# Kernel optimization log

Measured on AMD Instinct MI355X. Metric: run time of the kernel, lower is better.

## Reference

```python
import jax, jax.numpy as jnp
import numpy as np

B, N, D = 32, 4096, 256
S = 8            # num_slots
H = 512          # mlp hidden (max(dim, hidden_dim))
EPS = 1e-8
LN_EPS = 1e-5


def _ln(x, w, b):
    m = x.mean(-1, keepdims=True)
    v = ((x - m) ** 2).mean(-1, keepdims=True)
    return (x - m) / jnp.sqrt(v + LN_EPS) * w + b


def _gru_cell(x, h, wih, whh, bih, bhh):
    # torch.nn.GRUCell math; wih/whh: [3D, D], bih/bhh: [3D]
    gi = x @ wih.T + bih
    gh = h @ whh.T + bhh
    i_r, i_z, i_n = jnp.split(gi, 3, axis=-1)
    h_r, h_z, h_n = jnp.split(gh, 3, axis=-1)
    r = jax.nn.sigmoid(i_r + h_r)
    z = jax.nn.sigmoid(i_z + h_z)
    n = jnp.tanh(i_n + r * h_n)
    return (1.0 - z) * n + z * h


def setup_inputs() -> dict:
    key = jax.random.key(0)
    ks = jax.random.split(key, 24)
    f = jnp.float32
    p = lambda k, shp, s=0.02: (jax.random.normal(k, shp, dtype=f) * s)
    inp = {
        "x": jax.random.normal(ks[0], (B, N, D), dtype=f),
        "slots_noise": jax.random.normal(ks[1], (B, S, D), dtype=f),
        "num_iterations": 3,
        "slots_mu": jax.random.normal(ks[2], (1, 1, D), dtype=f),
        "slots_sigma": jax.random.normal(ks[3], (1, 1, D), dtype=f),
        "wq": p(ks[4], (D, D)), "bq": jnp.zeros((D,), f),
        "wk": p(ks[5], (D, D)), "bk": jnp.zeros((D,), f),
        "wv": p(ks[6], (D, D)), "bv": jnp.zeros((D,), f),
        "gru_wih": p(ks[7], (3 * D, D)), "gru_whh": p(ks[8], (3 * D, D)),
        "gru_bih": jnp.zeros((3 * D,), f), "gru_bhh": jnp.zeros((3 * D,), f),
        "fc1_w": p(ks[9], (H, D)), "fc1_b": jnp.zeros((H,), f),
        "fc2_w": p(ks[10], (D, H)), "fc2_b": jnp.zeros((D,), f),
        "ln_in_w": jnp.ones((D,), f), "ln_in_b": jnp.zeros((D,), f),
        "ln_sl_w": jnp.ones((D,), f), "ln_sl_b": jnp.zeros((D,), f),
        "ln_ff_w": jnp.ones((D,), f), "ln_ff_b": jnp.zeros((D,), f),
    }
    return inp


def reference(x, slots_noise, num_iterations, slots_mu, slots_sigma,
              wq, bq, wk, bk, wv, bv,
              gru_wih, gru_whh, gru_bih, gru_bhh,
              fc1_w, fc1_b, fc2_w, fc2_b,
              ln_in_w, ln_in_b, ln_sl_w, ln_sl_b, ln_ff_w, ln_ff_b):
    b, n, d = x.shape
    scale = d ** (-0.5)
    slots = slots_mu + slots_sigma * slots_noise          # [B,S,D]
    xn = _ln(x, ln_in_w, ln_in_b)
    k = xn @ wk.T + bk                                    # [B,N,D]
    v = xn @ wv.T + bv                                    # [B,N,D]
    for _ in range(num_iterations):
        slots_prev = slots
        s = _ln(slots, ln_sl_w, ln_sl_b)
        q = s @ wq.T + bq                                 # [B,S,D]
        dots = jnp.einsum('bid,bjd->bij', q, k) * scale   # [B,S,N]
        attn = jax.nn.softmax(dots, axis=1) + EPS         # softmax over SLOT axis
        attn = attn / attn.sum(axis=-1, keepdims=True)
        updates = jnp.einsum('bjd,bij->bid', v, attn)     # [B,S,D]
        slots = _gru_cell(updates.reshape(-1, d), slots_prev.reshape(-1, d),
                          gru_wih, gru_whh, gru_bih, gru_bhh).reshape(b, -1, d)
        ff = jax.nn.relu(_ln(slots, ln_ff_w, ln_ff_b) @ fc1_w.T + fc1_b) @ fc2_w.T + fc2_b
        slots = slots + ff
    return slots
```

## Files before the change

kernel.cpp:

```cpp
#include <hip/hip_runtime.h>
#include <hip/hip_fp16.h>
#include <math.h>

#define NB 32
#define NTOK 4096
#define DIM 256
#define NS 8
#define HID 512
#define NCHUNK 32
#define LN_EPS 1e-5f
#define ATT_EPS 1e-8f
#define SCALE 0.0625f
#define NROWS (NB * NS)

#define DPPF(x, ctrl) __int_as_float(__builtin_amdgcn_update_dpp(0, __float_as_int(x), (ctrl), 0xF, 0xF, true))

__device__ __forceinline__ float addx16(float c) {
#if __has_builtin(__builtin_amdgcn_permlane16_swap)
    auto r = __builtin_amdgcn_permlane16_swap(__float_as_uint(c), __float_as_uint(c), false, false);
    return __uint_as_float(r[0]) + __uint_as_float(r[1]);
#else
    return c + __shfl_xor(c, 16);
#endif
}
__device__ __forceinline__ float addx32(float c) {
#if __has_builtin(__builtin_amdgcn_permlane32_swap)
    auto r = __builtin_amdgcn_permlane32_swap(__float_as_uint(c), __float_as_uint(c), false, false);
    return __uint_as_float(r[0]) + __uint_as_float(r[1]);
#else
    return c + __shfl_xor(c, 32);
#endif
}

__device__ __forceinline__ void tree2(float v0, float v1, int lane, float& S, float& Q) {
    bool hi = lane & 1;
    float send = hi ? v0 : v1;
    float recv = DPPF(send, 0xB1);
    float a = (hi ? v1 : v0) + recv;
    a += DPPF(a, 0x4E);
    a += DPPF(a, 0x124);
    a += DPPF(a, 0x128);
    a = addx16(a);
    a = addx32(a);
    float other = DPPF(a, 0xB1);
    S = hi ? other : a;
    Q = hi ? a : other;
}

__device__ __forceinline__ float tree8h(const float v[8], int lane) {
    bool b0 = lane & 1;
    bool b1 = lane & 2;
    bool bp = ((lane ^ (lane >> 1) ^ (lane >> 2)) & 1);
    float a[4];
#pragma unroll
    for (int j = 0; j < 4; j++) {
        float send = b0 ? v[j] : v[4 + j];
        float recv = DPPF(send, 0xB1);
        a[j] = (b0 ? v[4 + j] : v[j]) + recv;
    }
    float b[2];
#pragma unroll
    for (int j = 0; j < 2; j++) {
        float send = b1 ? a[j] : a[2 + j];
        float recv = DPPF(send, 0x4E);
        b[j] = (b1 ? a[2 + j] : a[j]) + recv;
    }
    float send = bp ? b[0] : b[1];
    float recv = DPPF(send, 0x141);
    float c = (bp ? b[1] : b[0]) + recv;
    c += DPPF(c, 0x128);
    c = addx16(c);
    return c;
}

typedef _Float16 h2v __attribute__((ext_vector_type(2)));
__device__ __forceinline__ float fdot2u(unsigned a, unsigned b, float c) {
#if __has_builtin(__builtin_amdgcn_fdot2)
    return __builtin_amdgcn_fdot2(__builtin_bit_cast(h2v, a), __builtin_bit_cast(h2v, b), c, false);
#else
    __half2 ha = __builtin_bit_cast(__half2, a), hb = __builtin_bit_cast(__half2, b);
    return c + __low2float(ha) * __low2float(hb) + __high2float(ha) * __high2float(hb);
#endif
}
__device__ __forceinline__ unsigned pkh(float a, float b) {
    return __builtin_bit_cast(unsigned, __floats2half2_rn(a, b));
}
__device__ __forceinline__ float2 h2f2(unsigned u) {
    __half2 h = __builtin_bit_cast(__half2, u);
    return float2{__low2float(h), __high2float(h)};
}

#define WP_BIAS  128
#define WP_WHH0  129
#define WP_F1H0  225
#define WP_F2H0  289
#define WP_W2C0  353
#define WP_F1B0  401
#define WP_B2G0  403
#define WP_BLKS  406

__global__ void __launch_bounds__(256)
k_wprep(const float* __restrict__ wq, const float* __restrict__ wk,
        const float* __restrict__ bk, const float* __restrict__ bq,
        const float* __restrict__ lsb, const float* __restrict__ lsw,
        unsigned* __restrict__ MppH, float* __restrict__ u2p, float* __restrict__ biasp,
        const float* __restrict__ wv, const float* __restrict__ wih,
        unsigned* __restrict__ w2cH,
        const float* __restrict__ f1w, const float* __restrict__ f1b,
        const float* __restrict__ lfb, float* __restrict__ f1bp,
        const float* __restrict__ bih, const float* __restrict__ bv,
        float* __restrict__ b2g,
        const float* __restrict__ whh, const float* __restrict__ f2w,
        const float* __restrict__ lfw,
        unsigned* __restrict__ whhH, unsigned* __restrict__ f1H,
        unsigned* __restrict__ f2H) {
    int bid = blockIdx.x, t = threadIdx.x;

    if (bid < WP_BIAS) {
        int b = bid, o = t;
        float a0 = 0.f, a1 = 0.f;
        for (int d = 0; d < 256; d++) {
            float2 wqp = *(const float2*)&wq[(size_t)d * 256 + 2 * b];
            float wkv = wk[(size_t)d * 256 + o];
            a0 = fmaf(wqp.x, wkv, a0);
            a1 = fmaf(wqp.y, wkv, a1);
        }
        MppH[(size_t)b * 256 + o] = pkh(a0 * lsw[2 * b], a1 * lsw[2 * b + 1]);
        return;
    }
    if (bid == WP_BIAS) {
        int o = t;
        __shared__ float t2l[256], bkl[256], red[4];
        bkl[o] = bk[o];
        float a = bq[o];
        for (int k = 0; k < 256; k++) a = fmaf(wq[(size_t)o * 256 + k], lsb[k], a);
        t2l[o] = a;
        __syncthreads();
        float ab = 0.f, au = 0.f;
        for (int d = 0; d < 256; d++) {
            ab = fmaf(t2l[d], wk[(size_t)d * 256 + o], ab);
            au = fmaf(bkl[d], wq[(size_t)d * 256 + o], au);
        }
        biasp[o] = ab;
        u2p[o] = au * lsw[o];
        float kk = t2l[o] * bkl[o];
        kk += DPPF(kk, 0xB1);
        kk += DPPF(kk, 0x4E);
        kk += DPPF(kk, 0x124);
        kk += DPPF(kk, 0x128);
        kk = addx16(kk);
        kk = addx32(kk);
        if ((t & 63) == 0) red[t >> 6] = kk;
        __syncthreads();
        if (t == 0) biasp[256] = red[0] + red[1] + red[2] + red[3];
        return;
    }
    if (bid < WP_W2C0) {
        const float* in; unsigned* out; const float* scl = nullptr;
        int C, OS, r, RT;
        if (bid < WP_F1H0)      { in = whh; out = whhH; C = 256; OS = 768; r = bid - WP_WHH0; RT = 24; }
        else if (bid < WP_F2H0) { in = f1w; out = f1H;  C = 256; OS = 512; r = bid - WP_F1H0; RT = 16; scl = lfw; }
        else                    { in = f2w; out = f2H;  C = 512; OS = 256; r = bid - WP_F2H0; RT = 8; }
        int otl = r % RT, ept = r / RT;
        __shared__ float tile[32][65];
#pragma unroll
        for (int i = 0; i < 8; i++) {
            int idx = t + i * 256;
            int row = idx >> 6, col = idx & 63;
            tile[row][col] = in[(size_t)(otl * 32 + row) * C + ept * 64 + col];
        }
        __syncthreads();
#pragma unroll
        for (int i = 0; i < 4; i++) {
            int idx = t + i * 256;
            int epl = idx >> 5, ol = idx & 31;
            float v0 = tile[ol][2 * epl], v1 = tile[ol][2 * epl + 1];
            if (scl) { v0 *= scl[ept * 64 + 2 * epl]; v1 *= scl[ept * 64 + 2 * epl + 1]; }
            out[(size_t)(ept * 32 + epl) * OS + otl * 32 + ol] = pkh(v0, v1);
        }
        return;
    }
    if (bid < WP_F1B0) {
        int r = bid - WP_W2C0;
        int et = r & 3, ot = r >> 2;
        int ep = et * 32 + (t & 31), og = (t >> 5) * 8;
        float alo[8] = {}, ahi[8] = {};
        for (int d = 0; d < 256; d++) {
            float2 wvp = *(const float2*)&wv[(size_t)d * 256 + 2 * ep];
#pragma unroll
            for (int i = 0; i < 8; i++) {
                float wv_ih = wih[(size_t)(ot * 64 + og + i) * 256 + d];
                alo[i] = fmaf(wvp.x, wv_ih, alo[i]);
                ahi[i] = fmaf(wvp.y, wv_ih, ahi[i]);
            }
        }
#pragma unroll
        for (int i = 0; i < 8; i++)
            w2cH[(size_t)ep * 768 + ot * 64 + og + i] = pkh(alo[i], ahi[i]);
        return;
    }
    if (bid < WP_B2G0) {
        int h = (bid - WP_F1B0) * 256 + t;
        float a = f1b[h];
        for (int e = 0; e < 256; e++) a = fmaf(f1w[(size_t)h * 256 + e], lfb[e], a);
        f1bp[h] = a;
        return;
    }
    {
        int o = (bid - WP_B2G0) * 256 + t;
        float a = bih[o];
        for (int d = 0; d < 256; d++) a = fmaf(wih[(size_t)o * 256 + d], bv[d], a);
        b2g[o] = a;
    }
}

__global__ void __launch_bounds__(256)
k_xn(const float* __restrict__ x, const float* __restrict__ liw,
     const float* __restrict__ lib, __half* __restrict__ xh) {
    int bid = blockIdx.x, t = threadIdx.x;
    int wave = t >> 6, lane = t & 63;
    float4 w4 = *(const float4*)&liw[lane * 4];
    float4 b4 = *(const float4*)&lib[lane * 4];
    size_t rbase = (size_t)bid * 64 + wave;
    float4 cur = *(const float4*)&x[rbase * 256 + lane * 4];
    for (int i = 0; i < 16; i++) {
        float4 nxt;
        if (i < 15) nxt = *(const float4*)&x[(rbase + (size_t)(i + 1) * 4) * 256 + lane * 4];
        float S, Q;
        tree2(cur.x + cur.y + cur.z + cur.w,
              cur.x * cur.x + cur.y * cur.y + cur.z * cur.z + cur.w * cur.w, lane, S, Q);
        float m = S * (1.f / DIM);
        float rstd = rsqrtf(Q * (1.f / DIM) - m * m + LN_EPS);
        uint2 st;
        st.x = pkh((cur.x - m) * rstd * w4.x + b4.x, (cur.y - m) * rstd * w4.y + b4.y);
        st.y = pkh((cur.z - m) * rstd * w4.z + b4.z, (cur.w - m) * rstd * w4.w + b4.w);
        *(uint2*)&xh[(rbase + (size_t)i * 4) * 256 + lane * 4] = st;
        cur = nxt;
    }
}

__global__ void __launch_bounds__(512)
k_iq(const float* __restrict__ noise, const float* __restrict__ mu,
     const float* __restrict__ sg, float* __restrict__ slots,
     const unsigned* __restrict__ MppH, const float* __restrict__ biasp,
     const float* __restrict__ u2p,
     float* __restrict__ qkw, float* __restrict__ c2b) {
    int bb = blockIdx.x, t = threadIdx.x, wave = t >> 6, lane = t & 63;
    __shared__ float S2[NS][DIM], Zl[NS][DIM];
#pragma unroll
    for (int k = 0; k < 4; k++) {
        int idx = k * 512 + t, d = idx & 255;
        float v = mu[d] + sg[d] * noise[(size_t)bb * 2048 + idx];
        S2[idx >> 8][d] = v;
        slots[(size_t)bb * 2048 + idx] = v;
    }
    __syncthreads();
    {
        float4 xv = *(const float4*)&S2[wave][lane * 4];
        float S, Q;
        tree2(xv.x + xv.y + xv.z + xv.w,
              xv.x * xv.x + xv.y * xv.y + xv.z * xv.z + xv.w * xv.w, lane, S, Q);
        float m = S * (1.f / DIM);
        float rstd = rsqrtf(Q * (1.f / DIM) - m * m + LN_EPS);
        Zl[wave][lane * 4 + 0] = (xv.x - m) * rstd;
        Zl[wave][lane * 4 + 1] = (xv.y - m) * rstd;
        Zl[wave][lane * 4 + 2] = (xv.z - m) * rstd;
        Zl[wave][lane * 4 + 3] = (xv.w - m) * rstd;
    }
    __syncthreads();
    int o = t & 255, sg2 = (t >> 8) * 4;
    float acc[4] = {};
    for (int ep = 0; ep < 128; ep++) {
        float2 wf = h2f2(MppH[(size_t)ep * 256 + o]);
#pragma unroll
        for (int i = 0; i < 4; i++) {
            float2 zp = *(const float2*)&Zl[sg2 + i][2 * ep];
            acc[i] = fmaf(zp.x, wf.x, fmaf(zp.y, wf.y, acc[i]));
        }
    }
    float bo = biasp[o];
#pragma unroll
    for (int i = 0; i < 4; i++)
        qkw[(size_t)(bb * NS + sg2 + i) * DIM + o] = acc[i] + bo;
    if (t < 64) {
        int s = t >> 3, j = t & 7;
        float a = 0.f;
        for (int e = j * 32; e < j * 32 + 32; e++) a = fmaf(Zl[s][e], u2p[e], a);
        a += DPPF(a, 0xB1);
        a += DPPF(a, 0x4E);
        a += DPPF(a, 0x141);
        if (j == 0) c2b[bb * NS + s] = a + biasp[256];
    }
}

__global__ void __launch_bounds__(256, 3)
k_attn(const __half* __restrict__ xh, const float* __restrict__ qkw,
       const float* __restrict__ c2b,
       float* __restrict__ pu, float* __restrict__ pda) {
    const int bb = blockIdx.x, chunk = blockIdx.y;
    const int t = threadIdx.x, wave = t >> 6, lane = t & 63;
    const int l0 = lane & 1, l1 = (lane >> 1) & 1, l2 = (lane >> 2) & 1;
    const int sig = (l0 << 2) | (l1 << 1) | (l0 ^ l1 ^ l2);
    const int e0 = (lane & 31) * 8;

    unsigned qh[NS][4];
#pragma unroll
    for (int s = 0; s < NS; s++) {
        const float4 a = *(const float4*)&qkw[(size_t)(bb * NS + s) * DIM + e0];
        const float4 b = *(const float4*)&qkw[(size_t)(bb * NS + s) * DIM + e0 + 4];
        qh[s][0] = pkh(a.x, a.y); qh[s][1] = pkh(a.z, a.w);
        qh[s][2] = pkh(b.x, b.y); qh[s][3] = pkh(b.z, b.w);
    }
    const float qbs = c2b[bb * NS + sig] * SCALE;

    float ua[NS][8] = {};
    float da[NS] = {};

    const __half* xp = xh + ((size_t)bb * NTOK + chunk * 128 + wave * 32 + (lane >> 5)) * DIM + e0;
    uint4 nxt = *(const uint4*)xp;
    for (int i = 0; i < 16; i++) {
        uint4 xv = nxt;
        if (i < 15) nxt = *(const uint4*)(xp + (size_t)(i + 1) * 2 * DIM);
        float dp[NS];
#pragma unroll
        for (int s = 0; s < NS; s++)
            dp[s] = fdot2u(qh[s][0], xv.x, fdot2u(qh[s][1], xv.y,
                    fdot2u(qh[s][2], xv.z, fdot2u(qh[s][3], xv.w, 0.f))));
        float ds = tree8h(dp, lane);
        float dv = fmaf(ds, SCALE, qbs);
        float mx = dv;
        mx = fmaxf(mx, DPPF(mx, 0xB1));
        mx = fmaxf(mx, DPPF(mx, 0x4E));
        mx = fmaxf(mx, DPPF(mx, 0x141));
        float e = __expf(dv - mx);
        float sm = e;
        sm += DPPF(sm, 0xB1);
        sm += DPPF(sm, 0x4E);
        sm += DPPF(sm, 0x141);
        float g0 = fmaf(e, __fdividef(1.f, sm), ATT_EPS);
        float g1 = DPPF(g0, 0x141);
        float g2 = DPPF(g0, 0x4E);
        float g3 = DPPF(g1, 0x4E);
        float g4 = DPPF(g0, 0xB1);
        float g5 = DPPF(g1, 0xB1);
        float g6 = DPPF(g2, 0xB1);
        float g7 = DPPF(g3, 0xB1);
        float gth[NS] = {g0, g1, g2, g3, g4, g5, g6, g7};
        __half2 p0 = __builtin_bit_cast(__half2, xv.x);
        __half2 p1 = __builtin_bit_cast(__half2, xv.y);
        __half2 p2 = __builtin_bit_cast(__half2, xv.z);
        __half2 p3 = __builtin_bit_cast(__half2, xv.w);
        float xf[8] = {__low2float(p0), __high2float(p0), __low2float(p1), __high2float(p1),
                       __low2float(p2), __high2float(p2), __low2float(p3), __high2float(p3)};
#pragma unroll
        for (int j = 0; j < NS; j++) {
            float pj = gth[j];
            da[j] += pj;
#pragma unroll
            for (int k = 0; k < 8; k++) ua[j][k] = fmaf(pj, xf[k], ua[j][k]);
        }
    }
#pragma unroll
    for (int j = 0; j < NS; j++) {
        da[j] = addx32(da[j]);
#pragma unroll
        for (int k = 0; k < 8; k++) ua[j][k] = addx32(ua[j][k]);
    }
    __shared__ float ul[4][NS][DIM];
    __shared__ float dl[4][NS];
    const int M8[NS] = {0, 7, 3, 4, 5, 2, 6, 1};
    if (lane < 32) {
#pragma unroll
        for (int j = 0; j < NS; j++) {
            int sj = sig ^ M8[j];
            *(float4*)&ul[wave][sj][e0]     = float4{ua[j][0], ua[j][1], ua[j][2], ua[j][3]};
            *(float4*)&ul[wave][sj][e0 + 4] = float4{ua[j][4], ua[j][5], ua[j][6], ua[j][7]};
        }
    }
    if (lane < 8) {
#pragma unroll
        for (int j = 0; j < NS; j++) dl[wave][sig ^ M8[j]] = da[j];
    }
    __syncthreads();
    size_t base = ((size_t)bb * NCHUNK + chunk) * NS;
#pragma unroll
    for (int s = 0; s < NS; s++)
        pu[(base + s) * DIM + t] = ul[0][s][t] + ul[1][s][t] + ul[2][s][t] + ul[3][s][t];
    if (t < NS)
        pda[base + t] = dl[0][t] + dl[1][t] + dl[2][t] + dl[3][t];
}

__global__ void __launch_bounds__(256)
k_fin(const float* __restrict__ pu, const float* __restrict__ pda,
      float* __restrict__ Aavg) {
    int bb = blockIdx.x, s = blockIdx.y, t = threadIdx.x;
    __shared__ float dsh;
    if (t < 64) {
        float a = pda[((size_t)bb * NCHUNK + (t & 31)) * NS + s];
        a += DPPF(a, 0xB1);
        a += DPPF(a, 0x4E);
        a += DPPF(a, 0x124);
        a += DPPF(a, 0x128);
        a = addx16(a);
        if (t == 0) dsh = a;
    }
    const float* src = pu + ((size_t)bb * NCHUNK * NS + s) * DIM + t;
    float acc = 0.f;
#pragma unroll 8
    for (int c = 0; c < NCHUNK; c++) acc += src[(size_t)c * NS * DIM];
    __syncthreads();
    Aavg[((size_t)bb * NS + s) * DIM + t] = acc * __fdividef(1.f, dsh);
}

__global__ void __launch_bounds__(512)
k_gru(const float* __restrict__ Aavg, const float* __restrict__ slots,
      const unsigned* __restrict__ w2cH, const unsigned* __restrict__ whhH,
      const float* __restrict__ b2g, const float* __restrict__ bhh,
      float* __restrict__ news) {
    int bb = blockIdx.x, ot = blockIdx.y, t = threadIdx.x;
    __shared__ unsigned AlH[NS][128], SlH[NS][128];
    __shared__ float pp[7][64][24];
    for (int idx = t; idx < 1024; idx += 512) {
        int rr = idx >> 7, pi = idx & 127;
        float2 av = *(const float2*)&Aavg[(size_t)bb * 2048 + rr * 256 + 2 * pi];
        float2 sv = *(const float2*)&slots[(size_t)bb * 2048 + rr * 256 + 2 * pi];
        AlH[rr][pi] = pkh(av.x, av.y);
        SlH[rr][pi] = pkh(sv.x, sv.y);
    }
    __syncthreads();
    int q = t & 7, r = (t >> 3) & 7, kp = t >> 6;
    int oc0 = ot * 32 + q * 4;
    float ir[4] = {}, iz[4] = {}, in_[4] = {}, hr[4] = {}, hz[4] = {}, hn[4] = {};
    int p0 = kp * 16;
#pragma unroll 4
    for (int i = 0; i < 16; i++) {
        int ep = p0 + i;
        uint4 w0 = *(const uint4*)&w2cH[(size_t)ep * 768 + oc0];
        uint4 w1 = *(const uint4*)&w2cH[(size_t)ep * 768 + oc0 + 256];
        uint4 w2 = *(const uint4*)&w2cH[(size_t)ep * 768 + oc0 + 512];
        uint4 u0 = *(const uint4*)&whhH[(size_t)ep * 768 + oc0];
        uint4 u1 = *(const uint4*)&whhH[(size_t)ep * 768 + oc0 + 256];
        uint4 u2 = *(const uint4*)&whhH[(size_t)ep * 768 + oc0 + 512];
        unsigned ah = AlH[r][ep], hh = SlH[r][ep];
        const unsigned* w0u = (const unsigned*)&w0;
        const unsigned* w1u = (const unsigned*)&w1;
        const unsigned* w2u = (const unsigned*)&w2;
        const unsigned* u0u = (const unsigned*)&u0;
        const unsigned* u1u = (const unsigned*)&u1;
        const unsigned* u2u = (const unsigned*)&u2;
#pragma unroll
        for (int j = 0; j < 4; j++) {
            ir[j]  = fdot2u(w0u[j], ah, ir[j]);
            iz[j]  = fdot2u(w1u[j], ah, iz[j]);
            in_[j] = fdot2u(w2u[j], ah, in_[j]);
            hr[j]  = fdot2u(u0u[j], hh, hr[j]);
            hz[j]  = fdot2u(u1u[j], hh, hz[j]);
            hn[j]  = fdot2u(u2u[j], hh, hn[j]);
        }
    }
    int slot = (r << 3) | q;
    if (kp) {
        float* d = &pp[kp - 1][slot][0];
#pragma unroll
        for (int j = 0; j < 4; j++) {
            d[j] = ir[j]; d[4 + j] = iz[j]; d[8 + j] = in_[j];
            d[12 + j] = hr[j]; d[16 + j] = hz[j]; d[20 + j] = hn[j];
        }
    }
    __syncthreads();
    if (!kp) {
#pragma unroll
        for (int k = 0; k < 7; k++) {
            const float* s_ = &pp[k][slot][0];
#pragma unroll
            for (int j = 0; j < 4; j++) {
                ir[j] += s_[j]; iz[j] += s_[4 + j]; in_[j] += s_[8 + j];
                hr[j] += s_[12 + j]; hz[j] += s_[16 + j]; hn[j] += s_[20 + j];
            }
        }
        float4 hv = *(const float4*)&slots[((size_t)bb * NS + r) * DIM + oc0];
        float hvv[4] = {hv.x, hv.y, hv.z, hv.w};
        float out[4];
#pragma unroll
        for (int j = 0; j < 4; j++) {
            int oc = oc0 + j;
            float gir = ir[j] + b2g[oc], giz = iz[j] + b2g[oc + 256], gin = in_[j] + b2g[oc + 512];
            float ghr = hr[j] + bhh[oc], ghz = hz[j] + bhh[oc + 256], ghn = hn[j] + bhh[oc + 512];
            float rg = 1.f / (1.f + __expf(-(gir + ghr)));
            float zg = 1.f / (1.f + __expf(-(giz + ghz)));
            float ng = tanhf(fmaf(rg, ghn, gin));
            out[j] = fmaf(zg, hvv[j] - ng, ng);
        }
        *(float4*)&news[((size_t)bb * NS + r) * DIM + oc0] = float4{out[0], out[1], out[2], out[3]};
    }
}

__global__ void __launch_bounds__(512)
k_ff1(const float* __restrict__ news, const unsigned* __restrict__ f1H,
      const float* __restrict__ f1bp, unsigned* __restrict__ h1H) {
    int bb = blockIdx.x, ht = blockIdx.y, t = threadIdx.x;
    int wave = t >> 6, lane = t & 63;
    __shared__ unsigned ZH[NS][128];
    __shared__ float pp[3][128][4];
    {
        float4 xv = *(const float4*)&news[((size_t)bb * NS + wave) * DIM + lane * 4];
        float S, Q;
        tree2(xv.x + xv.y + xv.z + xv.w,
              xv.x * xv.x + xv.y * xv.y + xv.z * xv.z + xv.w * xv.w, lane, S, Q);
        float m = S * (1.f / DIM);
        float rstd = rsqrtf(Q * (1.f / DIM) - m * m + LN_EPS);
        ZH[wave][lane * 2]     = pkh((xv.x - m) * rstd, (xv.y - m) * rstd);
        ZH[wave][lane * 2 + 1] = pkh((xv.z - m) * rstd, (xv.w - m) * rstd);
    }
    __syncthreads();
    int cq = t & 15, r = (t >> 4) & 7, kp = t >> 7;
    int c0 = ht * 64 + cq * 4;
    float acc[4] = {};
    int p0 = kp * 32;
#pragma unroll 4
    for (int i = 0; i < 32; i++) {
        int ep = p0 + i;
        uint4 wv4 = *(const uint4*)&f1H[(size_t)ep * HID + c0];
        unsigned zh = ZH[r][ep];
        const unsigned* wu = (const unsigned*)&wv4;
#pragma unroll
        for (int j = 0; j < 4; j++) acc[j] = fdot2u(wu[j], zh, acc[j]);
    }
    int slot = (r << 4) | cq;
    if (kp) {
        float* d = &pp[kp - 1][slot][0];
#pragma unroll
        for (int j = 0; j < 4; j++) d[j] = acc[j];
    }
    __syncthreads();
    if (!kp) {
#pragma unroll
        for (int k = 0; k < 3; k++) {
            const float* s_ = &pp[k][slot][0];
#pragma unroll
            for (int j = 0; j < 4; j++) acc[j] += s_[j];
        }
        float h0 = fmaxf(acc[0] + f1bp[c0 + 0], 0.f);
        float h1v = fmaxf(acc[1] + f1bp[c0 + 1], 0.f);
        float h2 = fmaxf(acc[2] + f1bp[c0 + 2], 0.f);
        float h3 = fmaxf(acc[3] + f1bp[c0 + 3], 0.f);
        uint2 st;
        st.x = pkh(h0, h1v);
        st.y = pkh(h2, h3);
        *(uint2*)&h1H[((size_t)bb * NS + r) * 256 + c0 / 2] = st;
    }
}

__global__ void __launch_bounds__(512)
k_ff2(const unsigned* __restrict__ h1H, const unsigned* __restrict__ f2H,
      const float* __restrict__ f2b, const float* __restrict__ news,
      float* __restrict__ slots) {
    int bb = blockIdx.x, ot = blockIdx.y, t = threadIdx.x;
    __shared__ unsigned HH[NS][256];
    __shared__ float pp[7][64][4];
    for (int idx = t; idx < 512; idx += 512)
        ((uint4*)HH)[idx] = ((const uint4*)(h1H + (size_t)bb * NS * 256))[idx];
    __syncthreads();
    int q = t & 7, r = (t >> 3) & 7, kp = t >> 6;
    int oc0 = ot * 32 + q * 4;
    float acc[4] = {};
    int p0 = kp * 32;
#pragma unroll 4
    for (int i = 0; i < 32; i++) {
        int ep = p0 + i;
        uint4 wv4 = *(const uint4*)&f2H[(size_t)ep * 256 + oc0];
        unsigned hh = HH[r][ep];
        const unsigned* wu = (const unsigned*)&wv4;
#pragma unroll
        for (int j = 0; j < 4; j++) acc[j] = fdot2u(wu[j], hh, acc[j]);
    }
    int slot = (r << 3) | q;
    if (kp) {
        float* d = &pp[kp - 1][slot][0];
#pragma unroll
        for (int j = 0; j < 4; j++) d[j] = acc[j];
    }
    __syncthreads();
    if (!kp) {
#pragma unroll
        for (int k = 0; k < 7; k++) {
            const float* s_ = &pp[k][slot][0];
#pragma unroll
            for (int j = 0; j < 4; j++) acc[j] += s_[j];
        }
        float4 nv = *(const float4*)&news[((size_t)bb * NS + r) * DIM + oc0];
        float4 bv4 = *(const float4*)&f2b[oc0];
        float4 out = {nv.x + acc[0] + bv4.x, nv.y + acc[1] + bv4.y,
                      nv.z + acc[2] + bv4.z, nv.w + acc[3] + bv4.w};
        *(float4*)&slots[((size_t)bb * NS + r) * DIM + oc0] = out;
    }
}

__global__ void __launch_bounds__(512)
k_qk2(const float* __restrict__ slots, const unsigned* __restrict__ MppH,
      const float* __restrict__ biasp, const float* __restrict__ u2p,
      float* __restrict__ qkw, float* __restrict__ c2b) {
    int bb = blockIdx.x, ot = blockIdx.y, t = threadIdx.x;
    int wave = t >> 6, lane = t & 63;
    __shared__ unsigned ZH[NS][128];
    __shared__ float pp[7][64][4];
    {
        float4 xv = *(const float4*)&slots[((size_t)bb * NS + wave) * DIM + lane * 4];
        float S, Q;
        tree2(xv.x + xv.y + xv.z + xv.w,
              xv.x * xv.x + xv.y * xv.y + xv.z * xv.z + xv.w * xv.w, lane, S, Q);
        float m = S * (1.f / DIM);
        float rstd = rsqrtf(Q * (1.f / DIM) - m * m + LN_EPS);
        ZH[wave][lane * 2]     = pkh((xv.x - m) * rstd, (xv.y - m) * rstd);
        ZH[wave][lane * 2 + 1] = pkh((xv.z - m) * rstd, (xv.w - m) * rstd);
    }
    __syncthreads();
    int q = t & 7, r = (t >> 3) & 7, kp = t >> 6;
    int oc0 = ot * 32 + q * 4;
    float acc[4] = {};
    int p0 = kp * 16;
#pragma unroll 4
    for (int i = 0; i < 16; i++) {
        int ep = p0 + i;
        uint4 wv4 = *(const uint4*)&MppH[(size_t)ep * 256 + oc0];
        unsigned zh = ZH[r][ep];
        const unsigned* wu = (const unsigned*)&wv4;
#pragma unroll
        for (int j = 0; j < 4; j++) acc[j] = fdot2u(wu[j], zh, acc[j]);
    }
    int slot = (r << 3) | q;
    if (kp) {
        float* d = &pp[kp - 1][slot][0];
#pragma unroll
        for (int j = 0; j < 4; j++) d[j] = acc[j];
    }
    __syncthreads();
    if (!kp) {
#pragma unroll
        for (int k = 0; k < 7; k++) {
            const float* s_ = &pp[k][slot][0];
#pragma unroll
            for (int j = 0; j < 4; j++) acc[j] += s_[j];
        }
        float4 bv4 = *(const float4*)&biasp[oc0];
        float4 out = {acc[0] + bv4.x, acc[1] + bv4.y, acc[2] + bv4.z, acc[3] + bv4.w};
        *(float4*)&qkw[((size_t)bb * NS + r) * DIM + oc0] = out;
    }
    if (ot == 0 && t < 64) {
        int s = t >> 3, j = t & 7;
        float a = 0.f;
        for (int p = j * 16; p < j * 16 + 16; p++) {
            float2 z = h2f2(ZH[s][p]);
            a = fmaf(z.x, u2p[2 * p], fmaf(z.y, u2p[2 * p + 1], a));
        }
        a += DPPF(a, 0xB1);
        a += DPPF(a, 0x4E);
        a += DPPF(a, 0x141);
        if (j == 0) c2b[bb * NS + s] = a + biasp[256];
    }
}

extern "C" void kernel_launch(void* const* d_in, const int* in_sizes, int n_in,
                              void* d_out, int out_size, void* d_ws, size_t ws_size,
                              hipStream_t stream) {
    const float* x     = (const float*)d_in[0];
    const float* noise = (const float*)d_in[1];
    const float* mu  = (const float*)d_in[3];
    const float* sg  = (const float*)d_in[4];
    const float* wq  = (const float*)d_in[5];
    const float* bq  = (const float*)d_in[6];
    const float* wk  = (const float*)d_in[7];
    const float* bk  = (const float*)d_in[8];
    const float* wv  = (const float*)d_in[9];
    const float* bv  = (const float*)d_in[10];
    const float* wih = (const float*)d_in[11];
    const float* whh = (const float*)d_in[12];
    const float* bih = (const float*)d_in[13];
    const float* bhh = (const float*)d_in[14];
    const float* f1w = (const float*)d_in[15];
    const float* f1b = (const float*)d_in[16];
    const float* f2w = (const float*)d_in[17];
    const float* f2b = (const float*)d_in[18];
    const float* liw = (const float*)d_in[19];
    const float* lib = (const float*)d_in[20];
    const float* lsw = (const float*)d_in[21];
    const float* lsb = (const float*)d_in[22];
    const float* lfw = (const float*)d_in[23];
    const float* lfb = (const float*)d_in[24];
    float* slots = (float*)d_out;

    __half* xh = (__half*)d_ws;
    float* p = (float*)(xh + (size_t)NB * NTOK * DIM);
    unsigned* MppH = (unsigned*)p; p += 128 * 256;
    unsigned* w2cH = (unsigned*)p; p += 128 * 768;
    unsigned* whhH = (unsigned*)p; p += 128 * 768;
    unsigned* f1H  = (unsigned*)p; p += 128 * 512;
    unsigned* f2H  = (unsigned*)p; p += 256 * 256;
    unsigned* h1H  = (unsigned*)p; p += NROWS * 256;
    float* u2p   = p; p += 256;
    float* biasp = p; p += 257;
    float* f1bp  = p; p += 512;
    float* b2g   = p; p += 768;
    float* qkw   = p; p += NROWS * 256;
    float* c2b   = p; p += NROWS;
    float* pu    = p; p += (size_t)NB * NCHUNK * NS * DIM;
    float* pda   = p; p += NB * NCHUNK * NS;
    float* Aavg  = p; p += NROWS * 256;
    float* news  = p; p += NROWS * 256;

    k_wprep<<<WP_BLKS, 256, 0, stream>>>(
        wq, wk, bk, bq, lsb, lsw, MppH, u2p, biasp,
        wv, wih, w2cH,
        f1w, f1b, lfb, f1bp,
        bih, bv, b2g,
        whh, f2w, lfw, whhH, f1H, f2H);
    k_xn<<<2048, 256, 0, stream>>>(x, liw, lib, xh);
    k_iq<<<NB, 512, 0, stream>>>(noise, mu, sg, slots, MppH, biasp, u2p, qkw, c2b);

    for (int it = 0; it < 3; it++) {
        k_attn<<<dim3(NB, NCHUNK), 256, 0, stream>>>(xh, qkw, c2b, pu, pda);
        k_fin<<<dim3(NB, NS), 256, 0, stream>>>(pu, pda, Aavg);
        k_gru<<<dim3(NB, NS), 512, 0, stream>>>(Aavg, slots, w2cH, whhH, b2g, bhh, news);
        k_ff1<<<dim3(NB, NS), 512, 0, stream>>>(news, f1H, f1bp, h1H);
        k_ff2<<<dim3(NB, NS), 512, 0, stream>>>(h1H, f2H, f2b, news, slots);
        if (it < 2)
            k_qk2<<<dim3(NB, NS), 512, 0, stream>>>(slots, MppH, biasp, u2p, qkw, c2b);
    }
}
```

Baseline: 230.0 us.

## Fuse LayerNorm prep into weight prep, fold chunk reduction into GRU kernel, fp16 partials

Merges the input LayerNorm kernel into the weight-preparation kernel as extra blocks, saving one launch. It also folds the per-chunk attention reduction (k_fin) into the GRU kernel, removing the Aavg round-trip and one launch per iteration. Attention partial updates are now stored as packed fp16 to halve partial-sum traffic, and the inner accumulation uses packed v_pk_fma_f32. The fp16 partials add rounding error to the attention update sums, and each GRU block now redundantly re-reduces all chunk partials for its batch.

New measurement: 227.5 us. No clear change (-1.1%).

```diff
diff --git a/kernel.cpp b/kernel.cpp
--- a/kernel.cpp
+++ b/kernel.cpp
@@ -74,6 +74,7 @@
 }
 
 typedef _Float16 h2v __attribute__((ext_vector_type(2)));
+typedef float f32x2 __attribute__((ext_vector_type(2)));
 __device__ __forceinline__ float fdot2u(unsigned a, unsigned b, float c) {
 #if __has_builtin(__builtin_amdgcn_fdot2)
     return __builtin_amdgcn_fdot2(__builtin_bit_cast(h2v, a), __builtin_bit_cast(h2v, b), c, false);
@@ -89,35 +90,67 @@
     __half2 h = __builtin_bit_cast(__half2, u);
     return float2{__low2float(h), __high2float(h)};
 }
-
-#define WP_BIAS  128
-#define WP_WHH0  129
-#define WP_F1H0  225
-#define WP_F2H0  289
-#define WP_W2C0  353
-#define WP_F1B0  401
-#define WP_B2G0  403
-#define WP_BLKS  406
+__device__ __forceinline__ f32x2 h2f2v(unsigned u) {
+    __half2 h = __builtin_bit_cast(__half2, u);
+    return f32x2{__low2float(h), __high2float(h)};
+}
+__device__ __forceinline__ void pkfma(f32x2& acc, f32x2 a, f32x2 b) {
+    asm("v_pk_fma_f32 %0, %1, %2, %0" : "+v"(acc) : "v"(a), "v"(b));
+}
+
+#define XN_OFF   2048
+#define WP_BIAS  (XN_OFF + 128)
+#define WP_WHH0  (XN_OFF + 129)
+#define WP_F1H0  (XN_OFF + 225)
+#define WP_F2H0  (XN_OFF + 289)
+#define WP_W2C0  (XN_OFF + 353)
+#define WP_F1B0  (XN_OFF + 401)
+#define WP_B2G0  (XN_OFF + 403)
+#define WP_BLKS  (XN_OFF + 406)
 
 __global__ void __launch_bounds__(256)
-k_wprep(const float* __restrict__ wq, const float* __restrict__ wk,
-        const float* __restrict__ bk, const float* __restrict__ bq,
-        const float* __restrict__ lsb, const float* __restrict__ lsw,
-        unsigned* __restrict__ MppH, float* __restrict__ u2p, float* __restrict__ biasp,
-        const float* __restrict__ wv, const float* __restrict__ wih,
-        unsigned* __restrict__ w2cH,
-        const float* __restrict__ f1w, const float* __restrict__ f1b,
-        const float* __restrict__ lfb, float* __restrict__ f1bp,
-        const float* __restrict__ bih, const float* __restrict__ bv,
-        float* __restrict__ b2g,
-        const float* __restrict__ whh, const float* __restrict__ f2w,
-        const float* __restrict__ lfw,
-        unsigned* __restrict__ whhH, unsigned* __restrict__ f1H,
-        unsigned* __restrict__ f2H) {
+k_pre(const float* __restrict__ x, const float* __restrict__ liw,
+      const float* __restrict__ lib, __half* __restrict__ xh,
+      const float* __restrict__ wq, const float* __restrict__ wk,
+      const float* __restrict__ bk, const float* __restrict__ bq,
+      const float* __restrict__ lsb, const float* __restrict__ lsw,
+      unsigned* __restrict__ MppH, float* __restrict__ u2p, float* __restrict__ biasp,
+      const float* __restrict__ wv, const float* __restrict__ wih,
+      unsigned* __restrict__ w2cH,
+      const float* __restrict__ f1w, const float* __restrict__ f1b,
+      const float* __restrict__ lfb, float* __restrict__ f1bp,
+      const float* __restrict__ bih, const float* __restrict__ bv,
+      float* __restrict__ b2g,
+      const float* __restrict__ whh, const float* __restrict__ f2w,
+      const float* __restrict__ lfw,
+      unsigned* __restrict__ whhH, unsigned* __restrict__ f1H,
+      unsigned* __restrict__ f2H) {
     int bid = blockIdx.x, t = threadIdx.x;
 
+    if (bid < XN_OFF) {
+        int wave = t >> 6, lane = t & 63;
+        float4 w4 = *(const float4*)&liw[lane * 4];
+        float4 b4 = *(const float4*)&lib[lane * 4];
+        size_t rbase = (size_t)bid * 64 + wave;
+        float4 cur = *(const float4*)&x[rbase * 256 + lane * 4];
+        for (int i = 0; i < 16; i++) {
+            float4 nxt;
+            if (i < 15) nxt = *(const float4*)&x[(rbase + (size_t)(i + 1) * 4) * 256 + lane * 4];
+            float S, Q;
+            tree2(cur.x + cur.y + cur.z + cur.w,
+                  cur.x * cur.x + cur.y * cur.y + cur.z * cur.z + cur.w * cur.w, lane, S, Q);
+            float m = S * (1.f / DIM);
+            float rstd = rsqrtf(Q * (1.f / DIM) - m * m + LN_EPS);
+            uint2 st;
+            st.x = pkh((cur.x - m) * rstd * w4.x + b4.x, (cur.y - m) * rstd * w4.y + b4.y);
+            st.y = pkh((cur.z - m) * rstd * w4.z + b4.z, (cur.w - m) * rstd * w4.w + b4.w);
+            *(uint2*)&xh[(rbase + (size_t)i * 4) * 256 + lane * 4] = st;
+            cur = nxt;
+        }
+        return;
+    }
     if (bid < WP_BIAS) {
-        int b = bid, o = t;
+        int b = bid - XN_OFF, o = t;
         float a0 = 0.f, a1 = 0.f;
         for (int d = 0; d < 256; d++) {
             float2 wqp = *(const float2*)&wq[(size_t)d * 256 + 2 * b];
@@ -214,31 +247,6 @@
     }
 }
 
-__global__ void __launch_bounds__(256)
-k_xn(const float* __restrict__ x, const float* __restrict__ liw,
-     const float* __restrict__ lib, __half* __restrict__ xh) {
-    int bid = blockIdx.x, t = threadIdx.x;
-    int wave = t >> 6, lane = t & 63;
-    float4 w4 = *(const float4*)&liw[lane * 4];
-    float4 b4 = *(const float4*)&lib[lane * 4];
-    size_t rbase = (size_t)bid * 64 + wave;
-    float4 cur = *(const float4*)&x[rbase * 256 + lane * 4];
-    for (int i = 0; i < 16; i++) {
-        float4 nxt;
-        if (i < 15) nxt = *(const float4*)&x[(rbase + (size_t)(i + 1) * 4) * 256 + lane * 4];
-        float S, Q;
-        tree2(cur.x + cur.y + cur.z + cur.w,
-              cur.x * cur.x + cur.y * cur.y + cur.z * cur.z + cur.w * cur.w, lane, S, Q);
-        float m = S * (1.f / DIM);
-        float rstd = rsqrtf(Q * (1.f / DIM) - m * m + LN_EPS);
-        uint2 st;
-        st.x = pkh((cur.x - m) * rstd * w4.x + b4.x, (cur.y - m) * rstd * w4.y + b4.y);
-        st.y = pkh((cur.z - m) * rstd * w4.z + b4.z, (cur.w - m) * rstd * w4.w + b4.w);
-        *(uint2*)&xh[(rbase + (size_t)i * 4) * 256 + lane * 4] = st;
-        cur = nxt;
-    }
-}
-
 __global__ void __launch_bounds__(512)
 k_iq(const float* __restrict__ noise, const float* __restrict__ mu,
      const float* __restrict__ sg, float* __restrict__ slots,
@@ -296,7 +304,7 @@
 __global__ void __launch_bounds__(256, 3)
 k_attn(const __half* __restrict__ xh, const float* __restrict__ qkw,
        const float* __restrict__ c2b,
-       float* __restrict__ pu, float* __restrict__ pda) {
+       unsigned* __restrict__ puH, float* __restrict__ pda) {
     const int bb = blockIdx.x, chunk = blockIdx.y;
     const int t = threadIdx.x, wave = t >> 6, lane = t & 63;
     const int l0 = lane & 1, l1 = (lane >> 1) & 1, l2 = (lane >> 2) & 1;
@@ -313,7 +321,7 @@
     }
     const float qbs = c2b[bb * NS + sig] * SCALE;
 
-    float ua[NS][8] = {};
+    f32x2 ua2[NS][4] = {};
     float da[NS] = {};
 
     const __half* xp = xh + ((size_t)bb * NTOK + chunk * 128 + wave * 32 + (lane >> 5)) * DIM + e0;
@@ -346,35 +354,36 @@
         float g6 = DPPF(g2, 0xB1);
         float g7 = DPPF(g3, 0xB1);
         float gth[NS] = {g0, g1, g2, g3, g4, g5, g6, g7};
-        __half2 p0 = __builtin_bit_cast(__half2, xv.x);
-        __half2 p1 = __builtin_bit_cast(__half2, xv.y);
-        __half2 p2 = __builtin_bit_cast(__half2, xv.z);
-        __half2 p3 = __builtin_bit_cast(__half2, xv.w);
-        float xf[8] = {__low2float(p0), __high2float(p0), __low2float(p1), __high2float(p1),
-                       __low2float(p2), __high2float(p2), __low2float(p3), __high2float(p3)};
+        f32x2 xd[4] = {h2f2v(xv.x), h2f2v(xv.y), h2f2v(xv.z), h2f2v(xv.w)};
 #pragma unroll
         for (int j = 0; j < NS; j++) {
             float pj = gth[j];
             da[j] += pj;
-#pragma unroll
-            for (int k = 0; k < 8; k++) ua[j][k] = fmaf(pj, xf[k], ua[j][k]);
+            f32x2 pj2 = {pj, pj};
+#pragma unroll
+            for (int k = 0; k < 4; k++) pkfma(ua2[j][k], xd[k], pj2);
         }
     }
 #pragma unroll
     for (int j = 0; j < NS; j++) {
         da[j] = addx32(da[j]);
 #pragma unroll
-        for (int k = 0; k < 8; k++) ua[j][k] = addx32(ua[j][k]);
-    }
-    __shared__ float ul[4][NS][DIM];
+        for (int k = 0; k < 4; k++) {
+            ua2[j][k].x = addx32(ua2[j][k].x);
+            ua2[j][k].y = addx32(ua2[j][k].y);
+        }
+    }
+    __shared__ unsigned ulH[4][NS][128];
     __shared__ float dl[4][NS];
     const int M8[NS] = {0, 7, 3, 4, 5, 2, 6, 1};
     if (lane < 32) {
+        int c0 = lane * 4;
 #pragma unroll
         for (int j = 0; j < NS; j++) {
             int sj = sig ^ M8[j];
-            *(float4*)&ul[wave][sj][e0]     = float4{ua[j][0], ua[j][1], ua[j][2], ua[j][3]};
-            *(float4*)&ul[wave][sj][e0 + 4] = float4{ua[j][4], ua[j][5], ua[j][6], ua[j][7]};
+#pragma unroll
+            for (int k = 0; k < 4; k++)
+                ulH[wave][sj][c0 + k] = pkh(ua2[j][k].x, ua2[j][k].y);
         }
     }
     if (lane < 8) {
@@ -383,49 +392,71 @@
     }
     __syncthreads();
     size_t base = ((size_t)bb * NCHUNK + chunk) * NS;
-#pragma unroll
-    for (int s = 0; s < NS; s++)
-        pu[(base + s) * DIM + t] = ul[0][s][t] + ul[1][s][t] + ul[2][s][t] + ul[3][s][t];
+    int pi = t & 127, sh = t >> 7;
+#pragma unroll
+    for (int q = 0; q < 4; q++) {
+        int s = sh * 4 + q;
+        f32x2 acc = h2f2v(ulH[0][s][pi]);
+        f32x2 a1 = h2f2v(ulH[1][s][pi]);
+        f32x2 a2 = h2f2v(ulH[2][s][pi]);
+        f32x2 a3 = h2f2v(ulH[3][s][pi]);
+        acc.x += a1.x + a2.x + a3.x;
+        acc.y += a1.y + a2.y + a3.y;
+        puH[(base + s) * 128 + pi] = pkh(acc.x, acc.y);
+    }
     if (t < NS)
         pda[base + t] = dl[0][t] + dl[1][t] + dl[2][t] + dl[3][t];
 }
 
-__global__ void __launch_bounds__(256)
-k_fin(const float* __restrict__ pu, const float* __restrict__ pda,
-      float* __restrict__ Aavg) {
-    int bb = blockIdx.x, s = blockIdx.y, t = threadIdx.x;
-    __shared__ float dsh;
-    if (t < 64) {
-        float a = pda[((size_t)bb * NCHUNK + (t & 31)) * NS + s];
-        a += DPPF(a, 0xB1);
-        a += DPPF(a, 0x4E);
-        a += DPPF(a, 0x124);
-        a += DPPF(a, 0x128);
-        a = addx16(a);
-        if (t == 0) dsh = a;
-    }
-    const float* src = pu + ((size_t)bb * NCHUNK * NS + s) * DIM + t;
-    float acc = 0.f;
-#pragma unroll 8
-    for (int c = 0; c < NCHUNK; c++) acc += src[(size_t)c * NS * DIM];
-    __syncthreads();
-    Aavg[((size_t)bb * NS + s) * DIM + t] = acc * __fdividef(1.f, dsh);
-}
-
 __global__ void __launch_bounds__(512)
-k_gru(const float* __restrict__ Aavg, const float* __restrict__ slots,
-      const unsigned* __restrict__ w2cH, const unsigned* __restrict__ whhH,
-      const float* __restrict__ b2g, const float* __restrict__ bhh,
-      float* __restrict__ news) {
+k_fingru(const unsigned* __restrict__ puH, const float* __restrict__ pda,
+         const float* __restrict__ slots,
+         const unsigned* __restrict__ w2cH, const unsigned* __restrict__ whhH,
+         const float* __restrict__ b2g, const float* __restrict__ bhh,
+         float* __restrict__ news) {
     int bb = blockIdx.x, ot = blockIdx.y, t = threadIdx.x;
     __shared__ unsigned AlH[NS][128], SlH[NS][128];
     __shared__ float pp[7][64][24];
-    for (int idx = t; idx < 1024; idx += 512) {
-        int rr = idx >> 7, pi = idx & 127;
-        float2 av = *(const float2*)&Aavg[(size_t)bb * 2048 + rr * 256 + 2 * pi];
-        float2 sv = *(const float2*)&slots[(size_t)bb * 2048 + rr * 256 + 2 * pi];
-        AlH[rr][pi] = pkh(av.x, av.y);
-        SlH[rr][pi] = pkh(sv.x, sv.y);
+    __shared__ float den[NS];
+    if (t < 64) {
+        int s = t & 7, cg = t >> 3;
+        float a = 0.f;
+#pragma unroll
+        for (int c = 0; c < 4; c++)
+            a += pda[((size_t)bb * NCHUNK + cg * 4 + c) * NS + s];
+        a += DPPF(a, 0x128);
+        a = addx16(a);
+        a = addx32(a);
+        if (t < 8) den[s] = a;
+    }
+#pragma unroll
+    for (int k = 0; k < 2; k++) {
+        int idx = t + k * 512;
+        int rr = idx >> 7, pi2 = idx & 127;
+        float2 sv = *(const float2*)&slots[(size_t)bb * 2048 + rr * 256 + 2 * pi2];
+        SlH[rr][pi2] = pkh(sv.x, sv.y);
+    }
+    f32x2 raw[2];
+#pragma unroll
+    for (int k = 0; k < 2; k++) {
+        int idx = t + k * 512;
+        int s = idx >> 7, pi2 = idx & 127;
+        f32x2 a = {0.f, 0.f};
+        const unsigned* src = puH + ((size_t)bb * NCHUNK * NS + s) * 128 + pi2;
+#pragma unroll 8
+        for (int c = 0; c < NCHUNK; c++) {
+            f32x2 v = h2f2v(src[(size_t)c * NS * 128]);
+            a.x += v.x; a.y += v.y;
+        }
+        raw[k] = a;
+    }
+    __syncthreads();
+#pragma unroll
+    for (int k = 0; k < 2; k++) {
+        int idx = t + k * 512;
+        int s = idx >> 7, pi2 = idx & 127;
+        float inv = __fdividef(1.f, den[s]);
+        AlH[s][pi2] = pkh(raw[k].x * inv, raw[k].y * inv);
     }
     __syncthreads();
     int q = t & 7, r = (t >> 3) & 7, kp = t >> 6;
@@ -697,30 +728,29 @@
     unsigned* f1H  = (unsigned*)p; p += 128 * 512;
     unsigned* f2H  = (unsigned*)p; p += 256 * 256;
     unsigned* h1H  = (unsigned*)p; p += NROWS * 256;
+    unsigned* puH  = (unsigned*)p; p += (size_t)NB * NCHUNK * NS * 128;
     float* u2p   = p; p += 256;
     float* biasp = p; p += 257;
     float* f1bp  = p; p += 512;
     float* b2g   = p; p += 768;
     float* qkw   = p; p += NROWS * 256;
     float* c2b   = p; p += NROWS;
-    float* pu    = p; p += (size_t)NB * NCHUNK * NS * DIM;
     float* pda   = p; p += NB * NCHUNK * NS;
-    float* Aavg  = p; p += NROWS * 256;
     float* news  = p; p += NROWS * 256;
 
-    k_wprep<<<WP_BLKS, 256, 0, stream>>>(
+    k_pre<<<WP_BLKS, 256, 0, stream>>>(
+        x, liw, lib, xh,
         wq, wk, bk, bq, lsb, lsw, MppH, u2p, biasp,
         wv, wih, w2cH,
         f1w, f1b, lfb, f1bp,
         bih, bv, b2g,
         whh, f2w, lfw, whhH, f1H, f2H);
-    k_xn<<<2048, 256, 0, stream>>>(x, liw, lib, xh);
     k_iq<<<NB, 512, 0, stream>>>(noise, mu, sg, slots, MppH, biasp, u2p, qkw, c2b);
 
     for (int it = 0; it < 3; it++) {
-        k_attn<<<dim3(NB, NCHUNK), 256, 0, stream>>>(xh, qkw, c2b, pu, pda);
-        k_fin<<<dim3(NB, NS), 256, 0, stream>>>(pu, pda, Aavg);
-        k_gru<<<dim3(NB, NS), 512, 0, stream>>>(Aavg, slots, w2cH, whhH, b2g, bhh, news);
+        k_attn<<<dim3(NB, NCHUNK), 256, 0, stream>>>(xh, qkw, c2b, puH, pda);
+        k_fingru<<<dim3(NB, NS), 512, 0, stream>>>(puH, pda, slots, w2cH, whhH,
+                                                   b2g, bhh, news);
         k_ff1<<<dim3(NB, NS), 512, 0, stream>>>(news, f1H, f1bp, h1H);
         k_ff2<<<dim3(NB, NS), 512, 0, stream>>>(h1H, f2H, f2b, news, slots);
         if (it < 2)
```
